# Kernel optimization log

Hardware: AMD Instinct MI355X
Metric: run time of the kernel (lower is better)

## Reference

```python
import jax, jax.numpy as jnp
import numpy as np

B, T, E, H = 2, 2048, 1024, 16
D = E // H  # head_size

def setup_inputs() -> dict:
    key = jax.random.key(0)
    ks = jax.random.split(key, 6)
    s = 0.02
    return {
        "x":  jax.random.normal(ks[0], (B, T, E), dtype=jnp.float32),
        "Wq": jax.random.normal(ks[1], (E, E), dtype=jnp.float32) * s,
        "Wk": jax.random.normal(ks[2], (E, E), dtype=jnp.float32) * s,
        "Wv": jax.random.normal(ks[3], (E, E), dtype=jnp.float32) * s,
        "Wp": jax.random.normal(ks[4], (E, E), dtype=jnp.float32) * s,
        "bp": jnp.zeros((E,), dtype=jnp.float32),
    }

def reference(x, Wq, Wk, Wv, Wp, bp):
    b, t, e = x.shape
    # Per-head Linear(E, D, bias=False) stacked == single [E,E] matmul then head split.
    # torch Linear: y = x @ W.T
    q = (x @ Wq.T).reshape(b, t, H, D).transpose(0, 2, 1, 3)  # (B,H,T,D)
    k = (x @ Wk.T).reshape(b, t, H, D).transpose(0, 2, 1, 3)
    v = (x @ Wv.T).reshape(b, t, H, D).transpose(0, 2, 1, 3)
    scale = jnp.asarray(D, x.dtype) ** -0.5
    wei = jnp.einsum('bhqd,bhkd->bhqk', q, k) * scale  # (B,H,T,T)
    causal = jnp.tril(jnp.ones((t, t), dtype=bool))
    wei = jnp.where(causal, wei, -jnp.inf)
    wei = jax.nn.softmax(wei, axis=-1)
    # dropout p=0.0 -> identity (eval-mode determinism)
    out = jnp.einsum('bhqk,bhkd->bhqd', wei, v)  # (B,H,T,D)
    out = out.transpose(0, 2, 1, 3).reshape(b, t, e)  # concat heads
    return out @ Wp.T + bp
```

## Files before the change

### kernel.cpp

```cpp
#include <hip/hip_runtime.h>

#define T_ 2048
#define E_ 1024
#define H_ 16
#define D_ 64
#define M_ 4096

typedef unsigned short ushort_t;
typedef __attribute__((ext_vector_type(8))) short bf16x8;
typedef __attribute__((ext_vector_type(4))) float f32x4;
typedef __attribute__((ext_vector_type(8))) unsigned short u16x8;
typedef __attribute__((ext_vector_type(2))) unsigned int u32x2;

__device__ __forceinline__ ushort_t f2bf(float f) {
  union { float f; unsigned u; } v; v.f = f;
  unsigned r = v.u + 0x7FFFu + ((v.u >> 16) & 1u);
  return (ushort_t)(r >> 16);
}

__device__ __forceinline__ void gl16(const void* g, void* l) {
  __builtin_amdgcn_global_load_lds((const __attribute__((address_space(1))) void*)g,
                                   (__attribute__((address_space(3))) void*)l, 16, 0, 0);
}

__global__ __launch_bounds__(256)
void conv_all(const float* __restrict__ x,  const float* __restrict__ wq,
              const float* __restrict__ wk, const float* __restrict__ wv,
              const float* __restrict__ wp,
              ushort_t* __restrict__ xb,  ushort_t* __restrict__ wqb,
              ushort_t* __restrict__ wkb, ushort_t* __restrict__ wvb,
              ushort_t* __restrict__ wpb)
{
  const int id = blockIdx.x;
  const float* s; ushort_t* d; size_t off;
  if (id < 2048) { s = x; d = xb; off = (size_t)id * 2048; }
  else {
    int wsel = (id - 2048) >> 9, wid = (id - 2048) & 511;
    off = (size_t)wid * 2048;
    s = wsel == 0 ? wq : wsel == 1 ? wk : wsel == 2 ? wv : wp;
    d = wsel == 0 ? wqb : wsel == 1 ? wkb : wsel == 2 ? wvb : wpb;
  }
  size_t i = off + (size_t)threadIdx.x * 8;
  float4 a = *(const float4*)(s + i);
  float4 b = *(const float4*)(s + i + 4);
  u16x8 o;
  o[0]=f2bf(a.x); o[1]=f2bf(a.y); o[2]=f2bf(a.z); o[3]=f2bf(a.w);
  o[4]=f2bf(b.x); o[5]=f2bf(b.y); o[6]=f2bf(b.z); o[7]=f2bf(b.w);
  *(u16x8*)(d + i) = o;
}

__device__ __forceinline__ void gemm_core(const ushort_t* __restrict__ A,
                                          const ushort_t* __restrict__ W,
                                          int m0, int n0,
                                          ushort_t* As, ushort_t* Bs,
                                          f32x4 acc[4][4])
{
  const int t = threadIdx.x;
  const int lane = t & 63, w = t >> 6;
  const int g = lane >> 4, lq = lane & 15;
  const int wr = w >> 1, wc = w & 1;
  const int r0 = t >> 2;
  const int c0 = t & 3;
  const int ca0 = c0 ^ ((r0 >> 1) & 3);
  const int r1 = r0 + 64;
  const int ca1 = c0 ^ ((r1 >> 1) & 3);

  #pragma unroll
  for (int i = 0; i < 4; ++i)
    #pragma unroll
    for (int j = 0; j < 4; ++j) acc[i][j] = (f32x4){0.f,0.f,0.f,0.f};

  gl16(A + (size_t)(m0 + r0) * 1024 + ca0 * 8, As + t * 8);
  gl16(A + (size_t)(m0 + r1) * 1024 + ca1 * 8, As + 2048 + t * 8);
  gl16(W + (size_t)(n0 + r0) * 1024 + ca0 * 8, Bs + t * 8);
  gl16(W + (size_t)(n0 + r1) * 1024 + ca1 * 8, Bs + 2048 + t * 8);
  __syncthreads();

  int cur = 0;
  for (int k0 = 0; k0 < 1024; k0 += 32) {
    if (k0 + 32 < 1024) {
      const int nx = (cur ^ 1) * 4096;
      gl16(A + (size_t)(m0 + r0) * 1024 + k0 + 32 + ca0 * 8, As + nx + t * 8);
      gl16(A + (size_t)(m0 + r1) * 1024 + k0 + 32 + ca1 * 8, As + nx + 2048 + t * 8);
      gl16(W + (size_t)(n0 + r0) * 1024 + k0 + 32 + ca0 * 8, Bs + nx + t * 8);
      gl16(W + (size_t)(n0 + r1) * 1024 + k0 + 32 + ca1 * 8, Bs + nx + 2048 + t * 8);
    }
    const ushort_t* as = As + cur * 4096;
    const ushort_t* bs = Bs + cur * 4096;

    bf16x8 af[4], bfr[4];
    #pragma unroll
    for (int mi = 0; mi < 4; ++mi) {
      int row = wr * 64 + mi * 16 + lq;
      int ch = g ^ ((row >> 1) & 3);
      af[mi] = *(const bf16x8*)(as + row * 32 + ch * 8);
    }
    #pragma unroll
    for (int ni = 0; ni < 4; ++ni) {
      int row = wc * 64 + ni * 16 + lq;
      int ch = g ^ ((row >> 1) & 3);
      bfr[ni] = *(const bf16x8*)(bs + row * 32 + ch * 8);
    }
    __builtin_amdgcn_s_setprio(1);
    #pragma unroll
    for (int mi = 0; mi < 4; ++mi)
      #pragma unroll
      for (int ni = 0; ni < 4; ++ni)
        acc[mi][ni] = __builtin_amdgcn_mfma_f32_16x16x32_bf16(af[mi], bfr[ni], acc[mi][ni], 0, 0, 0);
    __builtin_amdgcn_s_setprio(0);

    __syncthreads();
    cur ^= 1;
  }
}

__global__ __launch_bounds__(256)
void gemm_qkv(const ushort_t* __restrict__ xb,
              const ushort_t* __restrict__ wqb, const ushort_t* __restrict__ wkb,
              const ushort_t* __restrict__ wvb,
              ushort_t* __restrict__ Qd, ushort_t* __restrict__ Kd, ushort_t* __restrict__ Vd)
{
  __shared__ __align__(16) ushort_t As[2 * 4096];
  __shared__ __align__(16) ushort_t Bs[2 * 4096];
  const int bx = blockIdx.x;
  const int sel = bx >> 3;
  const int n0 = (bx & 7) * 128;
  const int m0 = blockIdx.y * 128;
  const ushort_t* W = sel == 0 ? wqb : (sel == 1 ? wkb : wvb);
  f32x4 acc[4][4];
  gemm_core(xb, W, m0, n0, As, Bs, acc);

  const int t = threadIdx.x, lane = t & 63, w = t >> 6;
  const int g = lane >> 4, lq = lane & 15, wr = w >> 1, wc = w & 1;
  const float scl = (sel == 0) ? 0.125f : 1.0f;
  ushort_t* dst = sel == 0 ? Qd : (sel == 1 ? Kd : Vd);
  #pragma unroll
  for (int mi = 0; mi < 4; ++mi)
    #pragma unroll
    for (int ni = 0; ni < 4; ++ni)
      #pragma unroll
      for (int r = 0; r < 4; ++r) {
        int m = m0 + wr * 64 + mi * 16 + 4 * g + r;
        int n = n0 + wc * 64 + ni * 16 + lq;
        int b = m >> 11, tt = m & (T_ - 1);
        int h = n >> 6, d = n & (D_ - 1);
        ushort_t v = f2bf(acc[mi][ni][r] * scl);
        if (sel < 2) dst[((size_t)(b * H_ + h) * T_ + tt) * D_ + d] = v;
        else         dst[((size_t)(b * H_ + h) * D_ + d) * T_ + tt] = v;
      }
}

__global__ __launch_bounds__(256)
void gemm_out64(const ushort_t* __restrict__ Ab, const ushort_t* __restrict__ wpb,
                const float* __restrict__ bias, float* __restrict__ out)
{
  __shared__ __align__(16) ushort_t As[2 * 2048];
  __shared__ __align__(16) ushort_t Bs[2 * 4096];
  const int t = threadIdx.x, lane = t & 63, w = t >> 6;
  const int g = lane >> 4, lq = lane & 15;
  const int n0 = blockIdx.x * 128;
  const int m0 = blockIdx.y * 64;
  const int r0 = t >> 2, c0 = t & 3;
  const int ca0 = c0 ^ ((r0 >> 1) & 3);
  const int r1 = r0 + 64;
  const int ca1 = c0 ^ ((r1 >> 1) & 3);

  f32x4 acc[4][2];
  #pragma unroll
  for (int i = 0; i < 4; ++i) { acc[i][0] = (f32x4){0.f,0.f,0.f,0.f}; acc[i][1] = (f32x4){0.f,0.f,0.f,0.f}; }

  gl16(Ab  + (size_t)(m0 + r0) * 1024 + ca0 * 8, As + t * 8);
  gl16(wpb + (size_t)(n0 + r0) * 1024 + ca0 * 8, Bs + t * 8);
  gl16(wpb + (size_t)(n0 + r1) * 1024 + ca1 * 8, Bs + 2048 + t * 8);
  __syncthreads();

  int cur = 0;
  for (int k0 = 0; k0 < 1024; k0 += 32) {
    if (k0 + 32 < 1024) {
      gl16(Ab  + (size_t)(m0 + r0) * 1024 + k0 + 32 + ca0 * 8, As + (cur ^ 1) * 2048 + t * 8);
      gl16(wpb + (size_t)(n0 + r0) * 1024 + k0 + 32 + ca0 * 8, Bs + (cur ^ 1) * 4096 + t * 8);
      gl16(wpb + (size_t)(n0 + r1) * 1024 + k0 + 32 + ca1 * 8, Bs + (cur ^ 1) * 4096 + 2048 + t * 8);
    }
    const ushort_t* as = As + cur * 2048;
    const ushort_t* bs = Bs + cur * 4096;

    bf16x8 af[4], bfr[2];
    #pragma unroll
    for (int mi = 0; mi < 4; ++mi) {
      int row = mi * 16 + lq;
      int ch = g ^ ((row >> 1) & 3);
      af[mi] = *(const bf16x8*)(as + row * 32 + ch * 8);
    }
    #pragma unroll
    for (int ni = 0; ni < 2; ++ni) {
      int row = w * 32 + ni * 16 + lq;
      int ch = g ^ ((row >> 1) & 3);
      bfr[ni] = *(const bf16x8*)(bs + row * 32 + ch * 8);
    }
    __builtin_amdgcn_s_setprio(1);
    #pragma unroll
    for (int mi = 0; mi < 4; ++mi)
      #pragma unroll
      for (int ni = 0; ni < 2; ++ni)
        acc[mi][ni] = __builtin_amdgcn_mfma_f32_16x16x32_bf16(af[mi], bfr[ni], acc[mi][ni], 0, 0, 0);
    __builtin_amdgcn_s_setprio(0);

    __syncthreads();
    cur ^= 1;
  }
  #pragma unroll
  for (int mi = 0; mi < 4; ++mi)
    #pragma unroll
    for (int ni = 0; ni < 2; ++ni)
      #pragma unroll
      for (int r = 0; r < 4; ++r) {
        int m = m0 + mi * 16 + 4 * g + r;
        int n = n0 + w * 32 + ni * 16 + lq;
        out[(size_t)m * E_ + n] = acc[mi][ni][r] + bias[n];
      }
}

__global__ __launch_bounds__(256, 2)
void attn_mfma(const ushort_t* __restrict__ Q, const ushort_t* __restrict__ K,
               const ushort_t* __restrict__ Vt, ushort_t* __restrict__ O)
{
  __shared__ __align__(16) ushort_t Ks[2][4096];
  __shared__ __align__(16) ushort_t Vs[2][4096];
  __shared__ __align__(16) ushort_t Ps[128 * 72];
  const int t = threadIdx.x, w = t >> 6, lane = t & 63;
  const int g = lane >> 4, lq = lane & 15;
  const int i = blockIdx.x;
  const int p = i & 255;
  const int qt = 15 - (p >> 4);
  const int bh = ((p & 15) << 1) | (i >> 8);
  const int q0 = qt * 128;
  const size_t qkbase = (size_t)bh * T_ * D_;
  const size_t vbase  = (size_t)bh * D_ * T_;

  const int srow = t >> 3, sc = t & 7;
  const int cs0 = sc ^ (srow & 7);
  const int srow1 = srow + 32, cs1 = sc ^ (srow1 & 7);

  const int rowA = 32 * w + lq, rowB = rowA + 16;
  const int qgA = q0 + rowA, qgB = q0 + rowB;
  const bf16x8 qA0 = *(const bf16x8*)(Q + qkbase + (size_t)qgA * D_ + g * 8);
  const bf16x8 qA1 = *(const bf16x8*)(Q + qkbase + (size_t)qgA * D_ + 32 + g * 8);
  const bf16x8 qB0 = *(const bf16x8*)(Q + qkbase + (size_t)qgB * D_ + g * 8);
  const bf16x8 qB1 = *(const bf16x8*)(Q + qkbase + (size_t)qgB * D_ + 32 + g * 8);

  f32x4 accA[4], accB[4];
  #pragma unroll
  for (int db = 0; db < 4; ++db) { accA[db] = (f32x4){0.f,0.f,0.f,0.f}; accB[db] = (f32x4){0.f,0.f,0.f,0.f}; }
  float mA = -1e30f, lA = 0.f, mB = -1e30f, lB = 0.f;

  const int nt = 2 * qt + 2;

  gl16(K + qkbase + (size_t)srow  * D_ + cs0 * 8, &Ks[0][t * 8]);
  gl16(K + qkbase + (size_t)srow1 * D_ + cs1 * 8, &Ks[0][2048 + t * 8]);
  gl16(Vt + vbase + (size_t)srow  * T_ + cs0 * 8, &Vs[0][t * 8]);
  gl16(Vt + vbase + (size_t)srow1 * T_ + cs1 * 8, &Vs[0][2048 + t * 8]);
  asm volatile("s_waitcnt vmcnt(0)" ::: "memory");
  __builtin_amdgcn_s_barrier();

  for (int kt = 0; kt < nt; ++kt) {
    const int cur = kt & 1;
    const int k0 = kt * 64;
    if (kt + 1 < nt) {
      const int kn = (kt + 1) * 64;
      gl16(K + qkbase + (size_t)(kn + srow)  * D_ + cs0 * 8, &Ks[cur ^ 1][t * 8]);
      gl16(K + qkbase + (size_t)(kn + srow1) * D_ + cs1 * 8, &Ks[cur ^ 1][2048 + t * 8]);
      gl16(Vt + vbase + (size_t)srow  * T_ + kn + cs0 * 8, &Vs[cur ^ 1][t * 8]);
      gl16(Vt + vbase + (size_t)srow1 * T_ + kn + cs1 * 8, &Vs[cur ^ 1][2048 + t * 8]);
    }
    const ushort_t* kb_ = &Ks[cur][0];
    const ushort_t* vb_ = &Vs[cur][0];

    f32x4 stA[4], stB[4];
    __builtin_amdgcn_s_setprio(1);
    #pragma unroll
    for (int kb = 0; kb < 4; ++kb) {
      int krow = kb * 16 + lq;
      bf16x8 ka0 = *(const bf16x8*)(kb_ + krow * 64 + ((g ^ (krow & 7)) * 8));
      bf16x8 ka1 = *(const bf16x8*)(kb_ + krow * 64 + (((4 + g) ^ (krow & 7)) * 8));
      f32x4 zA = (f32x4){0.f,0.f,0.f,0.f};
      zA = __builtin_amdgcn_mfma_f32_16x16x32_bf16(ka0, qA0, zA, 0, 0, 0);
      zA = __builtin_amdgcn_mfma_f32_16x16x32_bf16(ka1, qA1, zA, 0, 0, 0);
      stA[kb] = zA;
      f32x4 zB = (f32x4){0.f,0.f,0.f,0.f};
      zB = __builtin_amdgcn_mfma_f32_16x16x32_bf16(ka0, qB0, zB, 0, 0, 0);
      zB = __builtin_amdgcn_mfma_f32_16x16x32_bf16(ka1, qB1, zB, 0, 0, 0);
      stB[kb] = zB;
    }
    __builtin_amdgcn_s_setprio(0);

    if (kt >= nt - 2) {
      #pragma unroll
      for (int kb = 0; kb < 4; ++kb)
        #pragma unroll
        for (int r = 0; r < 4; ++r) {
          int kg = k0 + kb * 16 + 4 * g + r;
          if (kg > qgA) stA[kb][r] = -1e30f;
          if (kg > qgB) stB[kb][r] = -1e30f;
        }
    }

    float tmA = -1e30f, tmB = -1e30f;
    #pragma unroll
    for (int kb = 0; kb < 4; ++kb)
      #pragma unroll
      for (int r = 0; r < 4; ++r) { tmA = fmaxf(tmA, stA[kb][r]); tmB = fmaxf(tmB, stB[kb][r]); }
    tmA = fmaxf(tmA, __shfl_xor(tmA, 16)); tmA = fmaxf(tmA, __shfl_xor(tmA, 32));
    tmB = fmaxf(tmB, __shfl_xor(tmB, 16)); tmB = fmaxf(tmB, __shfl_xor(tmB, 32));

    if (!__all((tmA <= mA + 8.f) && (tmB <= mB + 8.f))) {
      float mnA = fmaxf(mA, tmA), mnB = fmaxf(mB, tmB);
      float alA = __expf(mA - mnA), alB = __expf(mB - mnB);
      mA = mnA; mB = mnB;
      lA *= alA; lB *= alB;
      float alAr[4], alBr[4];
      #pragma unroll
      for (int r = 0; r < 4; ++r) { alAr[r] = __shfl(alA, 4 * g + r); alBr[r] = __shfl(alB, 4 * g + r); }
      #pragma unroll
      for (int db = 0; db < 4; ++db)
        #pragma unroll
        for (int r = 0; r < 4; ++r) { accA[db][r] *= alAr[r]; accB[db][r] *= alBr[r]; }
    }

    float tsA = 0.f, tsB = 0.f;
    #pragma unroll
    for (int kb = 0; kb < 4; ++kb) {
      float pA0 = __expf(stA[kb][0] - mA), pA1 = __expf(stA[kb][1] - mA);
      float pA2 = __expf(stA[kb][2] - mA), pA3 = __expf(stA[kb][3] - mA);
      float pB0 = __expf(stB[kb][0] - mB), pB1 = __expf(stB[kb][1] - mB);
      float pB2 = __expf(stB[kb][2] - mB), pB3 = __expf(stB[kb][3] - mB);
      tsA += (pA0 + pA1) + (pA2 + pA3);
      tsB += (pB0 + pB1) + (pB2 + pB3);
      unsigned aLo, aHi, bLo, bHi;
      asm("v_cvt_pk_bf16_f32 %0, %1, %2" : "=v"(aLo) : "v"(pA0), "v"(pA1));
      asm("v_cvt_pk_bf16_f32 %0, %1, %2" : "=v"(aHi) : "v"(pA2), "v"(pA3));
      asm("v_cvt_pk_bf16_f32 %0, %1, %2" : "=v"(bLo) : "v"(pB0), "v"(pB1));
      asm("v_cvt_pk_bf16_f32 %0, %1, %2" : "=v"(bHi) : "v"(pB2), "v"(pB3));
      *(u32x2*)(Ps + rowA * 72 + kb * 16 + 4 * g) = (u32x2){aLo, aHi};
      *(u32x2*)(Ps + rowB * 72 + kb * 16 + 4 * g) = (u32x2){bLo, bHi};
    }
    tsA += __shfl_xor(tsA, 16); tsA += __shfl_xor(tsA, 32);
    tsB += __shfl_xor(tsB, 16); tsB += __shfl_xor(tsB, 32);
    lA += tsA; lB += tsB;

    asm volatile("s_waitcnt lgkmcnt(0)" ::: "memory");
    bf16x8 paA0 = *(const bf16x8*)(Ps + rowA * 72 + g * 8);
    bf16x8 paA1 = *(const bf16x8*)(Ps + rowA * 72 + 32 + g * 8);
    bf16x8 paB0 = *(const bf16x8*)(Ps + rowB * 72 + g * 8);
    bf16x8 paB1 = *(const bf16x8*)(Ps + rowB * 72 + 32 + g * 8);

    __builtin_amdgcn_s_setprio(1);
    #pragma unroll
    for (int db = 0; db < 4; ++db) {
      int vrow = db * 16 + lq;
      bf16x8 vb0 = *(const bf16x8*)(vb_ + vrow * 64 + ((g ^ (vrow & 7)) * 8));
      bf16x8 vb1 = *(const bf16x8*)(vb_ + vrow * 64 + (((4 + g) ^ (vrow & 7)) * 8));
      accA[db] = __builtin_amdgcn_mfma_f32_16x16x32_bf16(paA0, vb0, accA[db], 0, 0, 0);
      accA[db] = __builtin_amdgcn_mfma_f32_16x16x32_bf16(paA1, vb1, accA[db], 0, 0, 0);
      accB[db] = __builtin_amdgcn_mfma_f32_16x16x32_bf16(paB0, vb0, accB[db], 0, 0, 0);
      accB[db] = __builtin_amdgcn_mfma_f32_16x16x32_bf16(paB1, vb1, accB[db], 0, 0, 0);
    }
    __builtin_amdgcn_s_setprio(0);

    if (kt + 1 < nt) asm volatile("s_waitcnt vmcnt(0)" ::: "memory");
    __builtin_amdgcn_s_barrier();
  }

  float invA = 1.0f / lA, invB = 1.0f / lB;
  float liA[4], liB[4];
  #pragma unroll
  for (int r = 0; r < 4; ++r) { liA[r] = __shfl(invA, 4 * g + r); liB[r] = __shfl(invB, 4 * g + r); }
  const int b = bh >> 4, h = bh & 15;
  #pragma unroll
  for (int db = 0; db < 4; ++db)
    #pragma unroll
    for (int r = 0; r < 4; ++r) {
      int mAo = q0 + 32 * w + 4 * g + r;
      int mBo = mAo + 16;
      O[((size_t)(b * T_ + mAo)) * E_ + h * 64 + db * 16 + lq] = f2bf(accA[db][r] * liA[r]);
      O[((size_t)(b * T_ + mBo)) * E_ + h * 64 + db * 16 + lq] = f2bf(accB[db][r] * liB[r]);
    }
}

extern "C" void kernel_launch(void* const* d_in, const int* in_sizes, int n_in,
                              void* d_out, int out_size, void* d_ws, size_t ws_size,
                              hipStream_t stream) {
  const float* x  = (const float*)d_in[0];
  const float* Wq = (const float*)d_in[1];
  const float* Wk = (const float*)d_in[2];
  const float* Wv = (const float*)d_in[3];
  const float* Wp = (const float*)d_in[4];
  const float* bp = (const float*)d_in[5];
  float* out = (float*)d_out;

  ushort_t* ws  = (ushort_t*)d_ws;
  ushort_t* xb  = ws;
  ushort_t* wqb = xb  + (size_t)M_ * E_;
  ushort_t* wkb = wqb + (size_t)E_ * E_;
  ushort_t* wvb = wkb + (size_t)E_ * E_;
  ushort_t* wpb = wvb + (size_t)E_ * E_;
  ushort_t* Qb  = wpb + (size_t)E_ * E_;
  ushort_t* Kb  = Qb  + (size_t)M_ * E_;
  ushort_t* Vb  = Kb  + (size_t)M_ * E_;
  ushort_t* Ab  = Vb  + (size_t)M_ * E_;

  conv_all<<<4096, 256, 0, stream>>>(x, Wq, Wk, Wv, Wp, xb, wqb, wkb, wvb, wpb);
  gemm_qkv<<<dim3(24, 32), 256, 0, stream>>>(xb, wqb, wkb, wvb, Qb, Kb, Vb);
  attn_mfma<<<512, 256, 0, stream>>>(Qb, Kb, Vb, Ab);
  gemm_out64<<<dim3(8, 64), 256, 0, stream>>>(Ab, wpb, bp, out);
}
```

Before: 130.2 us.

## Split attention KV range across two wave groups per block with LSE merge

The attention kernel now launches 512 threads per block, split into two groups of four waves. Each group processes half of the causal key tiles for the same 128-query tile, with its own double-buffered K/V and P shared-memory buffers. At the end, group 1 writes its partial accumulators and running max/sum to shared memory, and group 0 merges them with the usual online-softmax rescaling before writing the output. The aim is to shorten the serial KV loop per block and raise wave count per CU. The cost is more shared memory per block, an extra merge step, and a changed mapping from blocks to query tiles.

Result: faster. 114.4 us (median of 2 runs) (-12.1%).

```diff
diff --git a/kernel.cpp b/kernel.cpp
--- a/kernel.cpp
+++ b/kernel.cpp
@@ -220,28 +220,37 @@
       }
 }
 
-__global__ __launch_bounds__(256, 2)
+__global__ __launch_bounds__(512)
 void attn_mfma(const ushort_t* __restrict__ Q, const ushort_t* __restrict__ K,
                const ushort_t* __restrict__ Vt, ushort_t* __restrict__ O)
 {
-  __shared__ __align__(16) ushort_t Ks[2][4096];
-  __shared__ __align__(16) ushort_t Vs[2][4096];
-  __shared__ __align__(16) ushort_t Ps[128 * 72];
-  const int t = threadIdx.x, w = t >> 6, lane = t & 63;
+  __shared__ __align__(16) ushort_t Ks[2][2][4096];
+  __shared__ __align__(16) ushort_t Vs[2][2][4096];
+  __shared__ __align__(16) ushort_t Ps[2][128 * 72];
+  const int t = threadIdx.x;
+  const int w = t >> 6;
+  const int grp = w >> 2;
+  const int wl = w & 3;
+  const int tl = t & 255;
+  const int lane = t & 63;
   const int g = lane >> 4, lq = lane & 15;
   const int i = blockIdx.x;
-  const int p = i & 255;
-  const int qt = 15 - (p >> 4);
-  const int bh = ((p & 15) << 1) | (i >> 8);
+  int qt;
+  if (i < 256) qt = 15 - (i >> 5);
+  else         qt = 7 - ((i - 256) >> 5);
+  const int bh = i & 31;
   const int q0 = qt * 128;
   const size_t qkbase = (size_t)bh * T_ * D_;
   const size_t vbase  = (size_t)bh * D_ * T_;
 
-  const int srow = t >> 3, sc = t & 7;
+  const int srow = tl >> 3, sc = tl & 7;
   const int cs0 = sc ^ (srow & 7);
   const int srow1 = srow + 32, cs1 = sc ^ (srow1 & 7);
 
-  const int rowA = 32 * w + lq, rowB = rowA + 16;
+  const int nsteps = qt + 1;
+  const int ks = grp * nsteps;
+
+  const int rowA = 32 * wl + lq, rowB = rowA + 16;
   const int qgA = q0 + rowA, qgB = q0 + rowB;
   const bf16x8 qA0 = *(const bf16x8*)(Q + qkbase + (size_t)qgA * D_ + g * 8);
   const bf16x8 qA1 = *(const bf16x8*)(Q + qkbase + (size_t)qgA * D_ + 32 + g * 8);
@@ -253,27 +262,31 @@
   for (int db = 0; db < 4; ++db) { accA[db] = (f32x4){0.f,0.f,0.f,0.f}; accB[db] = (f32x4){0.f,0.f,0.f,0.f}; }
   float mA = -1e30f, lA = 0.f, mB = -1e30f, lB = 0.f;
 
-  const int nt = 2 * qt + 2;
-
-  gl16(K + qkbase + (size_t)srow  * D_ + cs0 * 8, &Ks[0][t * 8]);
-  gl16(K + qkbase + (size_t)srow1 * D_ + cs1 * 8, &Ks[0][2048 + t * 8]);
-  gl16(Vt + vbase + (size_t)srow  * T_ + cs0 * 8, &Vs[0][t * 8]);
-  gl16(Vt + vbase + (size_t)srow1 * T_ + cs1 * 8, &Vs[0][2048 + t * 8]);
+  ushort_t* Psg = &Ps[grp][0];
+
+  {
+    const int k0p = ks * 64;
+    gl16(K + qkbase + (size_t)(k0p + srow)  * D_ + cs0 * 8, &Ks[grp][0][tl * 8]);
+    gl16(K + qkbase + (size_t)(k0p + srow1) * D_ + cs1 * 8, &Ks[grp][0][2048 + tl * 8]);
+    gl16(Vt + vbase + (size_t)srow  * T_ + k0p + cs0 * 8, &Vs[grp][0][tl * 8]);
+    gl16(Vt + vbase + (size_t)srow1 * T_ + k0p + cs1 * 8, &Vs[grp][0][2048 + tl * 8]);
+  }
   asm volatile("s_waitcnt vmcnt(0)" ::: "memory");
   __builtin_amdgcn_s_barrier();
 
-  for (int kt = 0; kt < nt; ++kt) {
-    const int cur = kt & 1;
+  for (int s = 0; s < nsteps; ++s) {
+    const int kt = ks + s;
+    const int cur = s & 1;
     const int k0 = kt * 64;
-    if (kt + 1 < nt) {
+    if (s + 1 < nsteps) {
       const int kn = (kt + 1) * 64;
-      gl16(K + qkbase + (size_t)(kn + srow)  * D_ + cs0 * 8, &Ks[cur ^ 1][t * 8]);
-      gl16(K + qkbase + (size_t)(kn + srow1) * D_ + cs1 * 8, &Ks[cur ^ 1][2048 + t * 8]);
-      gl16(Vt + vbase + (size_t)srow  * T_ + kn + cs0 * 8, &Vs[cur ^ 1][t * 8]);
-      gl16(Vt + vbase + (size_t)srow1 * T_ + kn + cs1 * 8, &Vs[cur ^ 1][2048 + t * 8]);
-    }
-    const ushort_t* kb_ = &Ks[cur][0];
-    const ushort_t* vb_ = &Vs[cur][0];
+      gl16(K + qkbase + (size_t)(kn + srow)  * D_ + cs0 * 8, &Ks[grp][cur ^ 1][tl * 8]);
+      gl16(K + qkbase + (size_t)(kn + srow1) * D_ + cs1 * 8, &Ks[grp][cur ^ 1][2048 + tl * 8]);
+      gl16(Vt + vbase + (size_t)srow  * T_ + kn + cs0 * 8, &Vs[grp][cur ^ 1][tl * 8]);
+      gl16(Vt + vbase + (size_t)srow1 * T_ + kn + cs1 * 8, &Vs[grp][cur ^ 1][2048 + tl * 8]);
+    }
+    const ushort_t* kb_ = &Ks[grp][cur][0];
+    const ushort_t* vb_ = &Vs[grp][cur][0];
 
     f32x4 stA[4], stB[4];
     __builtin_amdgcn_s_setprio(1);
@@ -293,7 +306,7 @@
     }
     __builtin_amdgcn_s_setprio(0);
 
-    if (kt >= nt - 2) {
+    if (kt >= 2 * qt) {
       #pragma unroll
       for (int kb = 0; kb < 4; ++kb)
         #pragma unroll
@@ -340,18 +353,18 @@
       asm("v_cvt_pk_bf16_f32 %0, %1, %2" : "=v"(aHi) : "v"(pA2), "v"(pA3));
       asm("v_cvt_pk_bf16_f32 %0, %1, %2" : "=v"(bLo) : "v"(pB0), "v"(pB1));
       asm("v_cvt_pk_bf16_f32 %0, %1, %2" : "=v"(bHi) : "v"(pB2), "v"(pB3));
-      *(u32x2*)(Ps + rowA * 72 + kb * 16 + 4 * g) = (u32x2){aLo, aHi};
-      *(u32x2*)(Ps + rowB * 72 + kb * 16 + 4 * g) = (u32x2){bLo, bHi};
+      *(u32x2*)(Psg + rowA * 72 + kb * 16 + 4 * g) = (u32x2){aLo, aHi};
+      *(u32x2*)(Psg + rowB * 72 + kb * 16 + 4 * g) = (u32x2){bLo, bHi};
     }
     tsA += __shfl_xor(tsA, 16); tsA += __shfl_xor(tsA, 32);
     tsB += __shfl_xor(tsB, 16); tsB += __shfl_xor(tsB, 32);
     lA += tsA; lB += tsB;
 
     asm volatile("s_waitcnt lgkmcnt(0)" ::: "memory");
-    bf16x8 paA0 = *(const bf16x8*)(Ps + rowA * 72 + g * 8);
-    bf16x8 paA1 = *(const bf16x8*)(Ps + rowA * 72 + 32 + g * 8);
-    bf16x8 paB0 = *(const bf16x8*)(Ps + rowB * 72 + g * 8);
-    bf16x8 paB1 = *(const bf16x8*)(Ps + rowB * 72 + 32 + g * 8);
+    bf16x8 paA0 = *(const bf16x8*)(Psg + rowA * 72 + g * 8);
+    bf16x8 paA1 = *(const bf16x8*)(Psg + rowA * 72 + 32 + g * 8);
+    bf16x8 paB0 = *(const bf16x8*)(Psg + rowB * 72 + g * 8);
+    bf16x8 paB1 = *(const bf16x8*)(Psg + rowB * 72 + 32 + g * 8);
 
     __builtin_amdgcn_s_setprio(1);
     #pragma unroll
@@ -366,24 +379,63 @@
     }
     __builtin_amdgcn_s_setprio(0);
 
-    if (kt + 1 < nt) asm volatile("s_waitcnt vmcnt(0)" ::: "memory");
+    if (s + 1 < nsteps) asm volatile("s_waitcnt vmcnt(0)" ::: "memory");
     __builtin_amdgcn_s_barrier();
   }
 
-  float invA = 1.0f / lA, invB = 1.0f / lB;
-  float liA[4], liB[4];
-  #pragma unroll
-  for (int r = 0; r < 4; ++r) { liA[r] = __shfl(invA, 4 * g + r); liB[r] = __shfl(invB, 4 * g + r); }
-  const int b = bh >> 4, h = bh & 15;
-  #pragma unroll
-  for (int db = 0; db < 4; ++db)
+  float* accS = (float*)&Ks[0][0][0];
+  float* mlS  = (float*)&Vs[0][0][0];
+  if (grp == 1) {
+    #pragma unroll
+    for (int db = 0; db < 4; ++db)
+      #pragma unroll
+      for (int r = 0; r < 4; ++r) {
+        accS[tl * 32 + db * 4 + r]      = accA[db][r];
+        accS[tl * 32 + 16 + db * 4 + r] = accB[db][r];
+      }
+    mlS[tl * 4 + 0] = mA; mlS[tl * 4 + 1] = lA;
+    mlS[tl * 4 + 2] = mB; mlS[tl * 4 + 3] = lB;
+  }
+  asm volatile("s_waitcnt lgkmcnt(0)" ::: "memory");
+  __builtin_amdgcn_s_barrier();
+  if (grp == 0) {
+    const float m1A = mlS[tl * 4 + 0], l1A = mlS[tl * 4 + 1];
+    const float m1B = mlS[tl * 4 + 2], l1B = mlS[tl * 4 + 3];
+    const float moA = fmaxf(mA, m1A);
+    const float c0 = __expf(mA - moA), c1 = __expf(m1A - moA);
+    lA = lA * c0 + l1A * c1;
+    const float moB = fmaxf(mB, m1B);
+    const float d0 = __expf(mB - moB), d1 = __expf(m1B - moB);
+    lB = lB * d0 + l1B * d1;
+    float c0r[4], c1r[4], d0r[4], d1r[4];
     #pragma unroll
     for (int r = 0; r < 4; ++r) {
-      int mAo = q0 + 32 * w + 4 * g + r;
-      int mBo = mAo + 16;
-      O[((size_t)(b * T_ + mAo)) * E_ + h * 64 + db * 16 + lq] = f2bf(accA[db][r] * liA[r]);
-      O[((size_t)(b * T_ + mBo)) * E_ + h * 64 + db * 16 + lq] = f2bf(accB[db][r] * liB[r]);
-    }
+      c0r[r] = __shfl(c0, 4 * g + r); c1r[r] = __shfl(c1, 4 * g + r);
+      d0r[r] = __shfl(d0, 4 * g + r); d1r[r] = __shfl(d1, 4 * g + r);
+    }
+    #pragma unroll
+    for (int db = 0; db < 4; ++db)
+      #pragma unroll
+      for (int r = 0; r < 4; ++r) {
+        accA[db][r] = accA[db][r] * c0r[r] + accS[tl * 32 + db * 4 + r] * c1r[r];
+        accB[db][r] = accB[db][r] * d0r[r] + accS[tl * 32 + 16 + db * 4 + r] * d1r[r];
+      }
+
+    float invA = 1.0f / lA, invB = 1.0f / lB;
+    float liA[4], liB[4];
+    #pragma unroll
+    for (int r = 0; r < 4; ++r) { liA[r] = __shfl(invA, 4 * g + r); liB[r] = __shfl(invB, 4 * g + r); }
+    const int b = bh >> 4, h = bh & 15;
+    #pragma unroll
+    for (int db = 0; db < 4; ++db)
+      #pragma unroll
+      for (int r = 0; r < 4; ++r) {
+        int mAo = q0 + 32 * wl + 4 * g + r;
+        int mBo = mAo + 16;
+        O[((size_t)(b * T_ + mAo)) * E_ + h * 64 + db * 16 + lq] = f2bf(accA[db][r] * liA[r]);
+        O[((size_t)(b * T_ + mBo)) * E_ + h * 64 + db * 16 + lq] = f2bf(accB[db][r] * liB[r]);
+      }
+  }
 }
 
 extern "C" void kernel_launch(void* const* d_in, const int* in_sizes, int n_in,
@@ -410,6 +462,6 @@
 
   conv_all<<<4096, 256, 0, stream>>>(x, Wq, Wk, Wv, Wp, xb, wqb, wkb, wvb, wpb);
   gemm_qkv<<<dim3(24, 32), 256, 0, stream>>>(xb, wqb, wkb, wvb, Qb, Kb, Vb);
-  attn_mfma<<<512, 256, 0, stream>>>(Qb, Kb, Vb, Ab);
+  attn_mfma<<<512, 512, 0, stream>>>(Qb, Kb, Vb, Ab);
   gemm_out64<<<dim3(8, 64), 256, 0, stream>>>(Ab, wpb, bp, out);
 }
```
